# Kernel tuning notes

Hardware: AMD Instinct MI355X
Metric: run time of the kernel (lower is better)

Reference implementation:

```python
import jax, jax.numpy as jnp
import numpy as np

NUM_EXPERTS = 8
TOP_K = 2


def setup_inputs() -> dict:
    key = jax.random.key(0)
    k1, k2, k3, k4, k5 = jax.random.split(key, 5)
    B, S, D, I, E = 1, 2048, 1024, 2816, NUM_EXPERTS
    scale_in = 1.0 / np.sqrt(D)
    scale_mid = 1.0 / np.sqrt(I)
    return {
        "hidden_states": jax.random.normal(k1, (B, S, D), dtype=jnp.float32),
        "w_router": jax.random.normal(k2, (E, D), dtype=jnp.float32) * scale_in,
        "w_gate": jax.random.normal(k3, (E, D, I), dtype=jnp.float32) * scale_in,
        "w_up": jax.random.normal(k4, (E, D, I), dtype=jnp.float32) * scale_in,
        "w_down": jax.random.normal(k5, (E, I, D), dtype=jnp.float32) * scale_mid,
    }


def reference(hidden_states, w_router, w_gate, w_up, w_down):
    B, S, D = hidden_states.shape
    E, K = NUM_EXPERTS, TOP_K
    x = hidden_states.reshape(-1, D)  # (N, D)
    N = x.shape[0]

    # ---- TopKRouter ----
    router_logits = x @ w_router.T                                   # (N, E)
    router_probs = jax.nn.softmax(router_logits.astype(jnp.float32), axis=-1)
    expert_weights, expert_indices = jax.lax.top_k(router_probs, K)  # (N, K)
    # norm_topk_prob = True
    expert_weights = expert_weights / expert_weights.sum(axis=-1, keepdims=True)
    expert_weights = expert_weights.astype(x.dtype)

    # load-balancing aux loss (Switch formulation)
    one_hot = jax.nn.one_hot(expert_indices, E, dtype=jnp.float32)   # (N, K, E)
    tokens_per_expert = one_hot.sum(axis=(0, 1))                     # (E,)
    f = tokens_per_expert / (N * K)
    p = router_probs.mean(axis=0)
    aux_loss = E * jnp.sum(f * p)

    # ---- dropless dispatch/combine ----
    # combine weight per (token, expert): sum of routing weights over slots
    # assigned to that expert (zero for unrouted pairs -> same math as the
    # per-expert gather + index_add_ in the torch code).
    comb = jnp.einsum("nk,nke->ne", expert_weights, one_hot.astype(x.dtype))

    # SwiGLU expert FFN, batched over experts
    g = jnp.einsum("nd,edi->eni", x, w_gate)      # (E, N, I)
    u = jnp.einsum("nd,edi->eni", x, w_up)        # (E, N, I)
    h = jax.nn.silu(g) * u                         # (E, N, I)
    eo = jnp.einsum("eni,eid->end", h, w_down)    # (E, N, D)

    out = jnp.einsum("ne,end->nd", comb, eo)      # (N, D)
    return out.reshape(B, S, D), aux_loss
```

## Files before the change

### kernel.cpp

```cpp
#include <hip/hip_runtime.h>
#include <stdint.h>

#define N_TOK 2048
#define DM 1024
#define DI 2816
#define NE 8
#define NSLOT (N_TOK * 2)
#define BKP 72
#define MAXRT 40
#define NBLK (N_TOK / 4)

typedef __bf16 bf16x8 __attribute__((ext_vector_type(8)));
typedef float f32x4 __attribute__((ext_vector_type(4)));

__device__ __forceinline__ unsigned short f2bf(float f) {
    unsigned u = __builtin_bit_cast(unsigned, f);
    u += 0x7fffu + ((u >> 16) & 1u);
    return (unsigned short)(u >> 16);
}
__device__ __forceinline__ unsigned pack2bf(float a, float b) {
    return (unsigned)f2bf(a) | ((unsigned)f2bf(b) << 16);
}

__device__ __forceinline__ f32x4 mfma_bf16(bf16x8 a, bf16x8 b, f32x4 c) {
    return __builtin_amdgcn_mfma_f32_16x16x32_bf16(a, b, c, 0, 0, 0);
}

__global__ __launch_bounds__(256) void k_router(
    const float* __restrict__ x, const float* __restrict__ wr,
    float* __restrict__ probsum, int* __restrict__ te, float* __restrict__ tw,
    unsigned* __restrict__ hist)
{
    __shared__ int te_s[8];
    __shared__ float ps[4][NE];
    int w = threadIdx.x >> 6, lane = threadIdx.x & 63;
    int n = blockIdx.x * 4 + w;
    const float* xr = x + (size_t)n * DM;

    float acc[NE];
#pragma unroll
    for (int e = 0; e < NE; e++) acc[e] = 0.f;
#pragma unroll
    for (int it = 0; it < DM / 64; it++) {
        float xv = xr[lane + it * 64];
#pragma unroll
        for (int e = 0; e < NE; e++) acc[e] += xv * wr[e * DM + lane + it * 64];
    }
#pragma unroll
    for (int e = 0; e < NE; e++) {
        float v = acc[e];
#pragma unroll
        for (int off = 32; off; off >>= 1) v += __shfl_xor(v, off);
        acc[e] = v;
    }
    float m = acc[0];
#pragma unroll
    for (int e = 1; e < NE; e++) m = fmaxf(m, acc[e]);
    float p[NE], s = 0.f;
#pragma unroll
    for (int e = 0; e < NE; e++) { p[e] = __expf(acc[e] - m); s += p[e]; }
    float inv = 1.f / s;
#pragma unroll
    for (int e = 0; e < NE; e++) p[e] *= inv;
    int i0 = 0;
#pragma unroll
    for (int e = 1; e < NE; e++) if (p[e] > p[i0]) i0 = e;
    int i1 = (i0 == 0) ? 1 : 0;
#pragma unroll
    for (int e = 0; e < NE; e++) if (e != i0 && p[e] > p[i1]) i1 = e;
    float w0 = p[i0] / (p[i0] + p[i1]);
    float w1 = 1.f - w0;

    if (lane == 0) {
        te[2 * n] = i0; te[2 * n + 1] = i1;
        tw[2 * n] = w0; tw[2 * n + 1] = w1;
        te_s[2 * w] = i0; te_s[2 * w + 1] = i1;
    }
    if (lane < NE) ps[w][lane] = p[lane];
    __syncthreads();

    if (threadIdx.x < NE) {
        float s4 = ps[0][threadIdx.x] + ps[1][threadIdx.x] +
                   ps[2][threadIdx.x] + ps[3][threadIdx.x];
        atomicAdd(&probsum[threadIdx.x], s4);
    }
    if (w == 0) {
        unsigned v = 0;
        if (lane < NE) {
            int c = 0;
#pragma unroll
            for (int i = 0; i < 8; i++) c += (te_s[i] == lane);
            v = (unsigned)c << (4 * lane);
        }
        v |= __shfl_xor(v, 1); v |= __shfl_xor(v, 2); v |= __shfl_xor(v, 4);
        if (lane == 0) hist[blockIdx.x] = v;
    }
}

__global__ __launch_bounds__(512) void k_finalize(
    const unsigned* __restrict__ hist, const float* __restrict__ probsum,
    int* __restrict__ counts, int* __restrict__ base,
    int* __restrict__ nrt_out, unsigned short* __restrict__ rtmap,
    unsigned short* __restrict__ blockoff, float* __restrict__ aux_out)
{
    __shared__ int cnts_s[NE], base_s[NE];
    int tid = threadIdx.x;
    int e = tid >> 6, lane = tid & 63;

    int c[8], t = 0;
#pragma unroll
    for (int j = 0; j < 8; j++) {
        c[j] = (int)((hist[lane * 8 + j] >> (4 * e)) & 15u);
        t += c[j];
    }
    int incl = t;
#pragma unroll
    for (int off = 1; off < 64; off <<= 1) {
        int v = __shfl_up(incl, off);
        if (lane >= off) incl += v;
    }
    int excl = incl - t;
    if (lane == 63) cnts_s[e] = incl;
    __syncthreads();

    if (tid == 0) {
        int b = 0, nrt = 0; float aux = 0.f;
        for (int ee = 0; ee < NE; ee++) {
            int cc = cnts_s[ee];
            base_s[ee] = b;
            base[ee] = b;
            counts[ee] = cc;
            b += cc;
            aux += ((float)cc / (float)(N_TOK * 2)) *
                   (probsum[ee] / (float)N_TOK);
            int nt = (cc + 127) >> 7;
            for (int mt = 0; mt < nt; mt++)
                rtmap[nrt++] = (unsigned short)((ee << 8) | mt);
        }
        nrt_out[0] = nrt;
        aux_out[0] = aux * (float)NE;
    }
    __syncthreads();

    int run = base_s[e] + excl;
#pragma unroll
    for (int j = 0; j < 8; j++) {
        blockoff[(lane * 8 + j) * NE + e] = (unsigned short)run;
        run += c[j];
    }
}

__global__ __launch_bounds__(256) void k_gather(
    const float* __restrict__ x, const int* __restrict__ te,
    const unsigned short* __restrict__ blockoff,
    int* __restrict__ slots, unsigned short* __restrict__ Xg)
{
    __shared__ int te_s[8];
    int w = threadIdx.x >> 6, lane = threadIdx.x & 63;
    int n = blockIdx.x * 4 + w;
    if (lane == 0) {
        te_s[2 * w] = te[2 * n];
        te_s[2 * w + 1] = te[2 * n + 1];
    }
    __syncthreads();
    int s0 = 0, s1 = 0;
    if (lane == 0) {
        int i0 = 2 * w, i1 = 2 * w + 1;
        int e0 = te_s[i0], e1 = te_s[i1];
        int r0 = 0, r1 = 0;
        for (int j = 0; j < i0; j++) r0 += (te_s[j] == e0);
        for (int j = 0; j < i1; j++) r1 += (te_s[j] == e1);
        s0 = blockoff[blockIdx.x * NE + e0] + r0;
        s1 = blockoff[blockIdx.x * NE + e1] + r1;
        slots[2 * n] = s0; slots[2 * n + 1] = s1;
    }
    s0 = __shfl(s0, 0); s1 = __shfl(s1, 0);

    const float4* xr = (const float4*)(x + (size_t)n * DM);
    float4 f0 = xr[lane * 4 + 0], f1 = xr[lane * 4 + 1];
    float4 f2 = xr[lane * 4 + 2], f3 = xr[lane * 4 + 3];
    uint4 lo = make_uint4(pack2bf(f0.x, f0.y), pack2bf(f0.z, f0.w),
                          pack2bf(f1.x, f1.y), pack2bf(f1.z, f1.w));
    uint4 hi = make_uint4(pack2bf(f2.x, f2.y), pack2bf(f2.z, f2.w),
                          pack2bf(f3.x, f3.y), pack2bf(f3.z, f3.w));
    uint4* d0 = (uint4*)(Xg + (size_t)s0 * DM) + lane * 2;
    uint4* d1 = (uint4*)(Xg + (size_t)s1 * DM) + lane * 2;
    d0[0] = lo; d0[1] = hi;
    d1[0] = lo; d1[1] = hi;
}

__global__ __launch_bounds__(256) void k_pack(
    const float* __restrict__ src, unsigned short* __restrict__ dst,
    int R, int C)
{
    __shared__ unsigned short T[64][66];
    const float* s = src + (size_t)blockIdx.z * R * C;
    unsigned short* d = dst + (size_t)blockIdx.z * R * C;
    int r0 = blockIdx.y * 64, c0 = blockIdx.x * 64;
    int t = threadIdx.x;
    int ri = t >> 2, cc = (t & 3) * 16;
    const float4* sp = (const float4*)(s + (size_t)(r0 + ri) * C + c0 + cc);
    float4 f0 = sp[0], f1 = sp[1], f2 = sp[2], f3 = sp[3];
    unsigned short* tp = &T[ri][cc];
    *(unsigned*)(tp + 0)  = pack2bf(f0.x, f0.y);
    *(unsigned*)(tp + 2)  = pack2bf(f0.z, f0.w);
    *(unsigned*)(tp + 4)  = pack2bf(f1.x, f1.y);
    *(unsigned*)(tp + 6)  = pack2bf(f1.z, f1.w);
    *(unsigned*)(tp + 8)  = pack2bf(f2.x, f2.y);
    *(unsigned*)(tp + 10) = pack2bf(f2.z, f2.w);
    *(unsigned*)(tp + 12) = pack2bf(f3.x, f3.y);
    *(unsigned*)(tp + 14) = pack2bf(f3.z, f3.w);
    __syncthreads();
    int co = t >> 2, rr = (t & 3) * 16;
    unsigned w0 = (unsigned)T[rr + 0][co] | ((unsigned)T[rr + 1][co] << 16);
    unsigned w1 = (unsigned)T[rr + 2][co] | ((unsigned)T[rr + 3][co] << 16);
    unsigned w2 = (unsigned)T[rr + 4][co] | ((unsigned)T[rr + 5][co] << 16);
    unsigned w3 = (unsigned)T[rr + 6][co] | ((unsigned)T[rr + 7][co] << 16);
    unsigned w4 = (unsigned)T[rr + 8][co] | ((unsigned)T[rr + 9][co] << 16);
    unsigned w5 = (unsigned)T[rr + 10][co] | ((unsigned)T[rr + 11][co] << 16);
    unsigned w6 = (unsigned)T[rr + 12][co] | ((unsigned)T[rr + 13][co] << 16);
    unsigned w7 = (unsigned)T[rr + 14][co] | ((unsigned)T[rr + 15][co] << 16);
    unsigned short* dp = d + (size_t)(c0 + co) * R + r0 + rr;
    *(uint4*)(dp + 0) = make_uint4(w0, w1, w2, w3);
    *(uint4*)(dp + 8) = make_uint4(w4, w5, w6, w7);
}

template<bool PK>
__global__ __launch_bounds__(256, 4) void k_ffn1(
    const unsigned short* __restrict__ Xg,
    const float* __restrict__ wg, const float* __restrict__ wu,
    const unsigned short* __restrict__ wgp, const unsigned short* __restrict__ wup,
    const int* __restrict__ counts, const int* __restrict__ base,
    const int* __restrict__ nrt_p, const unsigned short* __restrict__ rtmap,
    unsigned short* __restrict__ H)
{
    __shared__ unsigned short As[128 * BKP];
    __shared__ unsigned short Bg[64 * BKP];
    __shared__ unsigned short Bu[64 * BKP];

    int tid = threadIdx.x;
    int w = tid >> 6, lane = tid & 63, quad = lane >> 4, ln = lane & 15;
    int ar = tid >> 1;
    int ak = (tid & 1) * 32;
    int kp = tid >> 3, n0 = (tid & 7) * 8;
    int kpsw2 = ((((kp >> 2) ^ (tid & 7)) << 2) | (kp & 3)) * 2;
    int nb = tid >> 2;
    int cA = (tid & 3) * 2;
    int boff0 = nb * BKP + ((cA ^ ((nb >> 3) & 7)) * 8);
    int boff1 = nb * BKP + (((cA + 1) ^ ((nb >> 3) & 7)) * 8);
    int bsrc = cA * 8;

    const int NCT = DI / 64;
    int total = nrt_p[0] * NCT;

    for (int tix = blockIdx.x; tix < total; tix += gridDim.x) {
        int rt = tix / NCT;
        int nc0 = (tix - rt * NCT) * 64;
        int em = rtmap[rt];
        int e = em >> 8, mt = em & 255;
        int cnt = counts[e];
        int row0 = base[e] + mt * 128;
        int rowEnd = base[e] + cnt;
        int arow = row0 + ar; if (arow > NSLOT - 1) arow = NSLOT - 1;

        f32x4 aG[2][4], aU[2][4];
        const f32x4 z = {0.f, 0.f, 0.f, 0.f};
#pragma unroll
        for (int i = 0; i < 2; i++)
#pragma unroll
            for (int j = 0; j < 4; j++) { aG[i][j] = z; aU[i][j] = z; }

        if constexpr (PK) {
            const unsigned short* wgpe = wgp + (size_t)e * DM * DI + (size_t)(nc0 + nb) * DM + bsrc;
            const unsigned short* wupe = wup + (size_t)e * DM * DI + (size_t)(nc0 + nb) * DM + bsrc;
            uint4 pa0, pa1, pa2, pa3, qg0, qg1, qu0, qu1;
            {
                const uint4* a_ = (const uint4*)(Xg + (size_t)arow * DM + ak);
                pa0 = a_[0]; pa1 = a_[1]; pa2 = a_[2]; pa3 = a_[3];
                qg0 = *(const uint4*)(wgpe);     qg1 = *(const uint4*)(wgpe + 8);
                qu0 = *(const uint4*)(wupe);     qu1 = *(const uint4*)(wupe + 8);
            }
            for (int kt = 0; kt < DM / 64; kt++) {
                *(uint4*)&As[ar * BKP + ak + 0]  = pa0;
                *(uint4*)&As[ar * BKP + ak + 8]  = pa1;
                *(uint4*)&As[ar * BKP + ak + 16] = pa2;
                *(uint4*)&As[ar * BKP + ak + 24] = pa3;
                *(uint4*)&Bg[boff0] = qg0;  *(uint4*)&Bg[boff1] = qg1;
                *(uint4*)&Bu[boff0] = qu0;  *(uint4*)&Bu[boff1] = qu1;
                __syncthreads();
                if (kt + 1 < DM / 64) {
                    int k0 = (kt + 1) * 64;
                    const uint4* a_ = (const uint4*)(Xg + (size_t)arow * DM + k0 + ak);
                    pa0 = a_[0]; pa1 = a_[1]; pa2 = a_[2]; pa3 = a_[3];
                    qg0 = *(const uint4*)(wgpe + k0);     qg1 = *(const uint4*)(wgpe + k0 + 8);
                    qu0 = *(const uint4*)(wupe + k0);     qu1 = *(const uint4*)(wupe + k0 + 8);
                }
#pragma unroll
                for (int s = 0; s < 2; s++) {
                    bf16x8 a0 = *(const bf16x8*)&As[(w * 32 + ln) * BKP + s * 32 + quad * 8];
                    bf16x8 a1 = *(const bf16x8*)&As[(w * 32 + 16 + ln) * BKP + s * 32 + quad * 8];
#pragma unroll
                    for (int j = 0; j < 4; j++) {
                        int nn = j * 16 + ln;
                        int grp = (s * 4 + quad) ^ ((nn >> 3) & 7);
                        bf16x8 bg = *(const bf16x8*)&Bg[nn * BKP + grp * 8];
                        bf16x8 bu = *(const bf16x8*)&Bu[nn * BKP + grp * 8];
                        aG[0][j] = mfma_bf16(a0, bg, aG[0][j]);
                        aG[1][j] = mfma_bf16(a1, bg, aG[1][j]);
                        aU[0][j] = mfma_bf16(a0, bu, aU[0][j]);
                        aU[1][j] = mfma_bf16(a1, bu, aU[1][j]);
                    }
                }
                __syncthreads();
            }
        } else {
            const float* wge = wg + (size_t)e * DM * DI;
            const float* wue = wu + (size_t)e * DM * DI;
            for (int kt = 0; kt < DM / 64; kt++) {
                int k0 = kt * 64;
                const uint4* asrc = (const uint4*)(Xg + (size_t)arow * DM + k0 + ak);
                uint4 av0 = asrc[0], av1 = asrc[1], av2 = asrc[2], av3 = asrc[3];
                const float* p0 = wge + (size_t)(k0 + 2 * kp) * DI + nc0 + n0;
                float4 g0 = *(const float4*)(p0),      g1 = *(const float4*)(p0 + 4);
                float4 g2 = *(const float4*)(p0 + DI), g3 = *(const float4*)(p0 + DI + 4);
                const float* p1 = wue + (size_t)(k0 + 2 * kp) * DI + nc0 + n0;
                float4 u0 = *(const float4*)(p1),      u1 = *(const float4*)(p1 + 4);
                float4 u2 = *(const float4*)(p1 + DI), u3 = *(const float4*)(p1 + DI + 4);
                *(uint4*)&As[ar * BKP + ak + 0]  = av0;
                *(uint4*)&As[ar * BKP + ak + 8]  = av1;
                *(uint4*)&As[ar * BKP + ak + 16] = av2;
                *(uint4*)&As[ar * BKP + ak + 24] = av3;
                unsigned short* bg = &Bg[n0 * BKP + kpsw2];
                unsigned short* bu = &Bu[n0 * BKP + kpsw2];
                *(unsigned*)(bg + 0 * BKP) = pack2bf(g0.x, g2.x);
                *(unsigned*)(bg + 1 * BKP) = pack2bf(g0.y, g2.y);
                *(unsigned*)(bg + 2 * BKP) = pack2bf(g0.z, g2.z);
                *(unsigned*)(bg + 3 * BKP) = pack2bf(g0.w, g2.w);
                *(unsigned*)(bg + 4 * BKP) = pack2bf(g1.x, g3.x);
                *(unsigned*)(bg + 5 * BKP) = pack2bf(g1.y, g3.y);
                *(unsigned*)(bg + 6 * BKP) = pack2bf(g1.z, g3.z);
                *(unsigned*)(bg + 7 * BKP) = pack2bf(g1.w, g3.w);
                *(unsigned*)(bu + 0 * BKP) = pack2bf(u0.x, u2.x);
                *(unsigned*)(bu + 1 * BKP) = pack2bf(u0.y, u2.y);
                *(unsigned*)(bu + 2 * BKP) = pack2bf(u0.z, u2.z);
                *(unsigned*)(bu + 3 * BKP) = pack2bf(u0.w, u2.w);
                *(unsigned*)(bu + 4 * BKP) = pack2bf(u1.x, u3.x);
                *(unsigned*)(bu + 5 * BKP) = pack2bf(u1.y, u3.y);
                *(unsigned*)(bu + 6 * BKP) = pack2bf(u1.z, u3.z);
                *(unsigned*)(bu + 7 * BKP) = pack2bf(u1.w, u3.w);
                __syncthreads();
#pragma unroll
                for (int s = 0; s < 2; s++) {
                    bf16x8 a0 = *(const bf16x8*)&As[(w * 32 + ln) * BKP + s * 32 + quad * 8];
                    bf16x8 a1 = *(const bf16x8*)&As[(w * 32 + 16 + ln) * BKP + s * 32 + quad * 8];
#pragma unroll
                    for (int j = 0; j < 4; j++) {
                        int nn = j * 16 + ln;
                        int grp = (s * 4 + quad) ^ ((nn >> 3) & 7);
                        bf16x8 bg8 = *(const bf16x8*)&Bg[nn * BKP + grp * 8];
                        bf16x8 bu8 = *(const bf16x8*)&Bu[nn * BKP + grp * 8];
                        aG[0][j] = mfma_bf16(a0, bg8, aG[0][j]);
                        aG[1][j] = mfma_bf16(a1, bg8, aG[1][j]);
                        aU[0][j] = mfma_bf16(a0, bu8, aU[0][j]);
                        aU[1][j] = mfma_bf16(a1, bu8, aU[1][j]);
                    }
                }
                __syncthreads();
            }
        }
#pragma unroll
        for (int i = 0; i < 2; i++)
#pragma unroll
            for (int r = 0; r < 4; r++) {
                int rl = w * 32 + i * 16 + quad * 4 + r;
                int grow = row0 + rl;
                if (grow < rowEnd) {
                    unsigned short* hp = H + (size_t)grow * DI + nc0 + ln;
#pragma unroll
                    for (int j = 0; j < 4; j++) {
                        float g = aG[i][j][r], u = aU[i][j][r];
                        float h = g * u / (1.f + __expf(-g));
                        hp[j * 16] = f2bf(h);
                    }
                }
            }
    }
}

template<bool PK>
__global__ __launch_bounds__(256, 4) void k_ffn2(
    const unsigned short* __restrict__ H, const float* __restrict__ wd,
    const unsigned short* __restrict__ wdp,
    const int* __restrict__ counts, const int* __restrict__ base,
    const int* __restrict__ nrt_p, const unsigned short* __restrict__ rtmap,
    float* __restrict__ O)
{
    __shared__ unsigned short As[128 * BKP];
    __shared__ unsigned short Bd[64 * BKP];

    int tid = threadIdx.x;
    int w = tid >> 6, lane = tid & 63, quad = lane >> 4, ln = lane & 15;
    int ar = tid >> 1;
    int ak = (tid & 1) * 32;
    int kp = tid >> 3, n0 = (tid & 7) * 8;
    int kpsw2 = ((((kp >> 2) ^ (tid & 7)) << 2) | (kp & 3)) * 2;
    int nb = tid >> 2;
    int cA = (tid & 3) * 2;
    int boff0 = nb * BKP + ((cA ^ ((nb >> 3) & 7)) * 8);
    int boff1 = nb * BKP + (((cA + 1) ^ ((nb >> 3) & 7)) * 8);
    int bsrc = cA * 8;

    const int NCT = DM / 64;
    int total = nrt_p[0] * NCT;

    for (int tix = blockIdx.x; tix < total; tix += gridDim.x) {
        int rt = tix >> 4;
        int nc0 = (tix & 15) * 64;
        int em = rtmap[rt];
        int e = em >> 8, mt = em & 255;
        int cnt = counts[e];
        int row0 = base[e] + mt * 128;
        int rowEnd = base[e] + cnt;
        int arow = row0 + ar; if (arow > NSLOT - 1) arow = NSLOT - 1;

        f32x4 acc[2][4];
        const f32x4 z = {0.f, 0.f, 0.f, 0.f};
#pragma unroll
        for (int i = 0; i < 2; i++)
#pragma unroll
            for (int j = 0; j < 4; j++) acc[i][j] = z;

        if constexpr (PK) {
            const unsigned short* wdpe = wdp + (size_t)e * DM * DI + (size_t)(nc0 + nb) * DI + bsrc;
            uint4 pa0, pa1, pa2, pa3, qd0, qd1;
            {
                const uint4* a_ = (const uint4*)(H + (size_t)arow * DI + ak);
                pa0 = a_[0]; pa1 = a_[1]; pa2 = a_[2]; pa3 = a_[3];
                qd0 = *(const uint4*)(wdpe);  qd1 = *(const uint4*)(wdpe + 8);
            }
            for (int kt = 0; kt < DI / 64; kt++) {
                *(uint4*)&As[ar * BKP + ak + 0]  = pa0;
                *(uint4*)&As[ar * BKP + ak + 8]  = pa1;
                *(uint4*)&As[ar * BKP + ak + 16] = pa2;
                *(uint4*)&As[ar * BKP + ak + 24] = pa3;
                *(uint4*)&Bd[boff0] = qd0;  *(uint4*)&Bd[boff1] = qd1;
                __syncthreads();
                if (kt + 1 < DI / 64) {
                    int k0 = (kt + 1) * 64;
                    const uint4* a_ = (const uint4*)(H + (size_t)arow * DI + k0 + ak);
                    pa0 = a_[0]; pa1 = a_[1]; pa2 = a_[2]; pa3 = a_[3];
                    qd0 = *(const uint4*)(wdpe + k0);  qd1 = *(const uint4*)(wdpe + k0 + 8);
                }
#pragma unroll
                for (int s = 0; s < 2; s++) {
                    bf16x8 a0 = *(const bf16x8*)&As[(w * 32 + ln) * BKP + s * 32 + quad * 8];
                    bf16x8 a1 = *(const bf16x8*)&As[(w * 32 + 16 + ln) * BKP + s * 32 + quad * 8];
#pragma unroll
                    for (int j = 0; j < 4; j++) {
                        int nn = j * 16 + ln;
                        int grp = (s * 4 + quad) ^ ((nn >> 3) & 7);
                        bf16x8 bd = *(const bf16x8*)&Bd[nn * BKP + grp * 8];
                        acc[0][j] = mfma_bf16(a0, bd, acc[0][j]);
                        acc[1][j] = mfma_bf16(a1, bd, acc[1][j]);
                    }
                }
                __syncthreads();
            }
        } else {
            const float* wde = wd + (size_t)e * DI * DM;
            for (int kt = 0; kt < DI / 64; kt++) {
                int k0 = kt * 64;
                const uint4* asrc = (const uint4*)(H + (size_t)arow * DI + k0 + ak);
                uint4 av0 = asrc[0], av1 = asrc[1], av2 = asrc[2], av3 = asrc[3];
                const float* p0 = wde + (size_t)(k0 + 2 * kp) * DM + nc0 + n0;
                float4 d0 = *(const float4*)(p0),      d1 = *(const float4*)(p0 + 4);
                float4 d2 = *(const float4*)(p0 + DM), d3 = *(const float4*)(p0 + DM + 4);
                *(uint4*)&As[ar * BKP + ak + 0]  = av0;
                *(uint4*)&As[ar * BKP + ak + 8]  = av1;
                *(uint4*)&As[ar * BKP + ak + 16] = av2;
                *(uint4*)&As[ar * BKP + ak + 24] = av3;
                unsigned short* bd = &Bd[n0 * BKP + kpsw2];
                *(unsigned*)(bd + 0 * BKP) = pack2bf(d0.x, d2.x);
                *(unsigned*)(bd + 1 * BKP) = pack2bf(d0.y, d2.y);
                *(unsigned*)(bd + 2 * BKP) = pack2bf(d0.z, d2.z);
                *(unsigned*)(bd + 3 * BKP) = pack2bf(d0.w, d2.w);
                *(unsigned*)(bd + 4 * BKP) = pack2bf(d1.x, d3.x);
                *(unsigned*)(bd + 5 * BKP) = pack2bf(d1.y, d3.y);
                *(unsigned*)(bd + 6 * BKP) = pack2bf(d1.z, d3.z);
                *(unsigned*)(bd + 7 * BKP) = pack2bf(d1.w, d3.w);
                __syncthreads();
#pragma unroll
                for (int s = 0; s < 2; s++) {
                    bf16x8 a0 = *(const bf16x8*)&As[(w * 32 + ln) * BKP + s * 32 + quad * 8];
                    bf16x8 a1 = *(const bf16x8*)&As[(w * 32 + 16 + ln) * BKP + s * 32 + quad * 8];
#pragma unroll
                    for (int j = 0; j < 4; j++) {
                        int nn = j * 16 + ln;
                        int grp = (s * 4 + quad) ^ ((nn >> 3) & 7);
                        bf16x8 bd8 = *(const bf16x8*)&Bd[nn * BKP + grp * 8];
                        acc[0][j] = mfma_bf16(a0, bd8, acc[0][j]);
                        acc[1][j] = mfma_bf16(a1, bd8, acc[1][j]);
                    }
                }
                __syncthreads();
            }
        }
#pragma unroll
        for (int i = 0; i < 2; i++)
#pragma unroll
            for (int r = 0; r < 4; r++) {
                int rl = w * 32 + i * 16 + quad * 4 + r;
                int grow = row0 + rl;
                if (grow < rowEnd) {
                    float* op = O + (size_t)grow * DM + nc0 + ln;
#pragma unroll
                    for (int j = 0; j < 4; j++) op[j * 16] = acc[i][j][r];
                }
            }
    }
}

__global__ __launch_bounds__(256) void k_combine(
    const float* __restrict__ O, const int* __restrict__ slots,
    const float* __restrict__ tw, float* __restrict__ out)
{
    int n = blockIdx.x;
    int s0 = slots[2 * n], s1 = slots[2 * n + 1];
    float w0 = tw[2 * n], w1 = tw[2 * n + 1];
    const float4* o0 = (const float4*)(O + (size_t)s0 * DM);
    const float4* o1 = (const float4*)(O + (size_t)s1 * DM);
    float4 a = o0[threadIdx.x], b = o1[threadIdx.x];
    float4 r;
    r.x = w0 * a.x + w1 * b.x;
    r.y = w0 * a.y + w1 * b.y;
    r.z = w0 * a.z + w1 * b.z;
    r.w = w0 * a.w + w1 * b.w;
    ((float4*)(out + (size_t)n * DM))[threadIdx.x] = r;
}

extern "C" void kernel_launch(void* const* d_in, const int* in_sizes, int n_in,
                              void* d_out, int out_size, void* d_ws, size_t ws_size,
                              hipStream_t stream)
{
    const float* x  = (const float*)d_in[0];
    const float* wr = (const float*)d_in[1];
    const float* wg = (const float*)d_in[2];
    const float* wu = (const float*)d_in[3];
    const float* wd = (const float*)d_in[4];
    float* out = (float*)d_out;

    char* ws = (char*)d_ws;
    int*   counts  = (int*)(ws + 0);
    float* probsum = (float*)(ws + 64);
    int*   base    = (int*)(ws + 96);
    int*   nrt     = (int*)(ws + 128);
    unsigned short* rtmap = (unsigned short*)(ws + 132);
    int*   te      = (int*)(ws + 256);
    float* tw      = (float*)(ws + 256 + 16384);
    int*   slots   = (int*)(ws + 256 + 32768);

    size_t off_Xg = 49408;
    size_t off_Hb = off_Xg + (size_t)NSLOT * DM * 2;
    size_t off_O  = off_Hb + (size_t)NSLOT * DI * 2;
    size_t off_Wg = off_O + (size_t)NSLOT * DM * 4;
    size_t off_Wu = off_Wg + (size_t)NE * DM * DI * 2;
    size_t off_Wd = off_Wu + (size_t)NE * DM * DI * 2;
    size_t end_GU = off_Wd;
    size_t end_D  = off_Wd + (size_t)NE * DM * DI * 2;

    unsigned short* Xg  = (unsigned short*)(ws + off_Xg);
    unsigned short* Hb  = (unsigned short*)(ws + off_Hb);
    float*          O   = (float*)(ws + off_O);
    unsigned short* Wgp = (unsigned short*)(ws + off_Wg);
    unsigned short* Wup = (unsigned short*)(ws + off_Wu);
    unsigned short* Wdp = (unsigned short*)(ws + off_Wd);

    unsigned*       hist     = (unsigned*)(ws + off_O);
    unsigned short* blockoff = (unsigned short*)(ws + off_O + 4096);

    bool pkGU = ws_size >= end_GU;
    bool pkD  = ws_size >= end_D;

    hipMemsetAsync(ws, 0, 128, stream);
    k_router<<<NBLK, 256, 0, stream>>>(x, wr, probsum, te, tw, hist);
    k_finalize<<<1, 512, 0, stream>>>(hist, probsum, counts, base, nrt, rtmap,
                                      blockoff, out + (size_t)N_TOK * DM);
    k_gather<<<NBLK, 256, 0, stream>>>(x, te, blockoff, slots, Xg);

    if (pkGU) {
        k_pack<<<dim3(DI / 64, DM / 64, NE), 256, 0, stream>>>(wg, Wgp, DM, DI);
        k_pack<<<dim3(DI / 64, DM / 64, NE), 256, 0, stream>>>(wu, Wup, DM, DI);
    }
    if (pkD)
        k_pack<<<dim3(DM / 64, DI / 64, NE), 256, 0, stream>>>(wd, Wdp, DI, DM);

    if (pkGU)
        k_ffn1<true><<<MAXRT * (DI / 64), 256, 0, stream>>>(
            Xg, wg, wu, Wgp, Wup, counts, base, nrt, rtmap, Hb);
    else
        k_ffn1<false><<<MAXRT * (DI / 64), 256, 0, stream>>>(
            Xg, wg, wu, Wgp, Wup, counts, base, nrt, rtmap, Hb);

    if (pkD)
        k_ffn2<true><<<MAXRT * (DM / 64), 256, 0, stream>>>(
            Hb, wd, Wdp, counts, base, nrt, rtmap, O);
    else
        k_ffn2<false><<<MAXRT * (DM / 64), 256, 0, stream>>>(
            Hb, wd, Wdp, counts, base, nrt, rtmap, O);

    k_combine<<<N_TOK, 256, 0, stream>>>(O, slots, tw, out);
}
```

Before: 465.5 us.

## Fuse gate/up weight packing and remap FFN tile order for XCD locality

Merges the two gate/up weight pack launches into one grid with a doubled z dimension, saving a launch and its tail. In both FFN kernels the tile index now runs over row tiles fastest within each column tile. Block IDs are also remapped so that each group of consecutive block IDs (round-robined across the 8 XCDs) lands on a contiguous tile range. The aim is that blocks sharing a weight column tile run on the same XCD and reuse its L2, at the cost of an extra integer divide per tile.

```diff
diff --git a/kernel.cpp b/kernel.cpp
--- a/kernel.cpp
+++ b/kernel.cpp
@@ -189,13 +189,10 @@
     d1[0] = lo; d1[1] = hi;
 }
 
-__global__ __launch_bounds__(256) void k_pack(
-    const float* __restrict__ src, unsigned short* __restrict__ dst,
-    int R, int C)
+__device__ __forceinline__ void pack_body(
+    const float* __restrict__ s, unsigned short* __restrict__ d, int R, int C)
 {
     __shared__ unsigned short T[64][66];
-    const float* s = src + (size_t)blockIdx.z * R * C;
-    unsigned short* d = dst + (size_t)blockIdx.z * R * C;
     int r0 = blockIdx.y * 64, c0 = blockIdx.x * 64;
     int t = threadIdx.x;
     int ri = t >> 2, cc = (t & 3) * 16;
@@ -225,6 +222,25 @@
     *(uint4*)(dp + 8) = make_uint4(w4, w5, w6, w7);
 }
 
+__global__ __launch_bounds__(256) void k_pack(
+    const float* __restrict__ src, unsigned short* __restrict__ dst,
+    int R, int C)
+{
+    pack_body(src + (size_t)blockIdx.z * R * C,
+              dst + (size_t)blockIdx.z * R * C, R, C);
+}
+
+__global__ __launch_bounds__(256) void k_pack2(
+    const float* __restrict__ srcA, unsigned short* __restrict__ dstA,
+    const float* __restrict__ srcB, unsigned short* __restrict__ dstB,
+    int R, int C)
+{
+    int z = blockIdx.z;
+    const float* s = (z < NE ? srcA : srcB) + (size_t)(z & 7) * R * C;
+    unsigned short* d = (z < NE ? dstA : dstB) + (size_t)(z & 7) * R * C;
+    pack_body(s, d, R, C);
+}
+
 template<bool PK>
 __global__ __launch_bounds__(256, 4) void k_ffn1(
     const unsigned short* __restrict__ Xg,
@@ -251,11 +267,14 @@
     int bsrc = cA * 8;
 
     const int NCT = DI / 64;
-    int total = nrt_p[0] * NCT;
-
-    for (int tix = blockIdx.x; tix < total; tix += gridDim.x) {
-        int rt = tix / NCT;
-        int nc0 = (tix - rt * NCT) * 64;
+    int nrt_v = nrt_p[0];
+    int total = nrt_v * NCT;
+    int wgid = (blockIdx.x & 7) * (gridDim.x >> 3) + (blockIdx.x >> 3);
+
+    for (int tix = wgid; tix < total; tix += gridDim.x) {
+        int nc = tix / nrt_v;
+        int rt = tix - nc * nrt_v;
+        int nc0 = nc * 64;
         int em = rtmap[rt];
         int e = em >> 8, mt = em & 255;
         int cnt = counts[e];
@@ -411,11 +430,14 @@
     int bsrc = cA * 8;
 
     const int NCT = DM / 64;
-    int total = nrt_p[0] * NCT;
-
-    for (int tix = blockIdx.x; tix < total; tix += gridDim.x) {
-        int rt = tix >> 4;
-        int nc0 = (tix & 15) * 64;
+    int nrt_v = nrt_p[0];
+    int total = nrt_v * NCT;
+    int wgid = (blockIdx.x & 7) * (gridDim.x >> 3) + (blockIdx.x >> 3);
+
+    for (int tix = wgid; tix < total; tix += gridDim.x) {
+        int nc = tix / nrt_v;
+        int rt = tix - nc * nrt_v;
+        int nc0 = nc * 64;
         int em = rtmap[rt];
         int e = em >> 8, mt = em & 255;
         int cnt = counts[e];
@@ -587,10 +609,9 @@
                                       blockoff, out + (size_t)N_TOK * DM);
     k_gather<<<NBLK, 256, 0, stream>>>(x, te, blockoff, slots, Xg);
 
-    if (pkGU) {
-        k_pack<<<dim3(DI / 64, DM / 64, NE), 256, 0, stream>>>(wg, Wgp, DM, DI);
-        k_pack<<<dim3(DI / 64, DM / 64, NE), 256, 0, stream>>>(wu, Wup, DM, DI);
-    }
+    if (pkGU)
+        k_pack2<<<dim3(DI / 64, DM / 64, 2 * NE), 256, 0, stream>>>(
+            wg, Wgp, wu, Wup, DM, DI);
     if (pkD)
         k_pack<<<dim3(DM / 64, DI / 64, NE), 256, 0, stream>>>(wd, Wdp, DI, DM);
 
```

Measured after the change: 474.1 us. About the same (+1.8%).

## Drop weight pre-pack kernels and convert fp32 weights inside the GEMM loops

Applied to the files above, without the earlier changes.

Removes the three k_pack launches that transposed and converted the gate, up and down weights to bf16 in the workspace, along with the templated packed paths. The FFN kernels now always read fp32 weights directly and convert them to bf16 while staging into shared memory. This avoids a full extra read and write pass over all expert weights on every call. In exchange, each GEMM tile reads twice the bytes and loses the register prefetch double-buffering the packed path had.

```diff
diff --git a/kernel.cpp b/kernel.cpp
--- a/kernel.cpp
+++ b/kernel.cpp
@@ -189,47 +189,9 @@
     d1[0] = lo; d1[1] = hi;
 }
 
-__global__ __launch_bounds__(256) void k_pack(
-    const float* __restrict__ src, unsigned short* __restrict__ dst,
-    int R, int C)
-{
-    __shared__ unsigned short T[64][66];
-    const float* s = src + (size_t)blockIdx.z * R * C;
-    unsigned short* d = dst + (size_t)blockIdx.z * R * C;
-    int r0 = blockIdx.y * 64, c0 = blockIdx.x * 64;
-    int t = threadIdx.x;
-    int ri = t >> 2, cc = (t & 3) * 16;
-    const float4* sp = (const float4*)(s + (size_t)(r0 + ri) * C + c0 + cc);
-    float4 f0 = sp[0], f1 = sp[1], f2 = sp[2], f3 = sp[3];
-    unsigned short* tp = &T[ri][cc];
-    *(unsigned*)(tp + 0)  = pack2bf(f0.x, f0.y);
-    *(unsigned*)(tp + 2)  = pack2bf(f0.z, f0.w);
-    *(unsigned*)(tp + 4)  = pack2bf(f1.x, f1.y);
-    *(unsigned*)(tp + 6)  = pack2bf(f1.z, f1.w);
-    *(unsigned*)(tp + 8)  = pack2bf(f2.x, f2.y);
-    *(unsigned*)(tp + 10) = pack2bf(f2.z, f2.w);
-    *(unsigned*)(tp + 12) = pack2bf(f3.x, f3.y);
-    *(unsigned*)(tp + 14) = pack2bf(f3.z, f3.w);
-    __syncthreads();
-    int co = t >> 2, rr = (t & 3) * 16;
-    unsigned w0 = (unsigned)T[rr + 0][co] | ((unsigned)T[rr + 1][co] << 16);
-    unsigned w1 = (unsigned)T[rr + 2][co] | ((unsigned)T[rr + 3][co] << 16);
-    unsigned w2 = (unsigned)T[rr + 4][co] | ((unsigned)T[rr + 5][co] << 16);
-    unsigned w3 = (unsigned)T[rr + 6][co] | ((unsigned)T[rr + 7][co] << 16);
-    unsigned w4 = (unsigned)T[rr + 8][co] | ((unsigned)T[rr + 9][co] << 16);
-    unsigned w5 = (unsigned)T[rr + 10][co] | ((unsigned)T[rr + 11][co] << 16);
-    unsigned w6 = (unsigned)T[rr + 12][co] | ((unsigned)T[rr + 13][co] << 16);
-    unsigned w7 = (unsigned)T[rr + 14][co] | ((unsigned)T[rr + 15][co] << 16);
-    unsigned short* dp = d + (size_t)(c0 + co) * R + r0 + rr;
-    *(uint4*)(dp + 0) = make_uint4(w0, w1, w2, w3);
-    *(uint4*)(dp + 8) = make_uint4(w4, w5, w6, w7);
-}
-
-template<bool PK>
 __global__ __launch_bounds__(256, 4) void k_ffn1(
     const unsigned short* __restrict__ Xg,
     const float* __restrict__ wg, const float* __restrict__ wu,
-    const unsigned short* __restrict__ wgp, const unsigned short* __restrict__ wup,
     const int* __restrict__ counts, const int* __restrict__ base,
     const int* __restrict__ nrt_p, const unsigned short* __restrict__ rtmap,
     unsigned short* __restrict__ H)
@@ -244,11 +206,6 @@
     int ak = (tid & 1) * 32;
     int kp = tid >> 3, n0 = (tid & 7) * 8;
     int kpsw2 = ((((kp >> 2) ^ (tid & 7)) << 2) | (kp & 3)) * 2;
-    int nb = tid >> 2;
-    int cA = (tid & 3) * 2;
-    int boff0 = nb * BKP + ((cA ^ ((nb >> 3) & 7)) * 8);
-    int boff1 = nb * BKP + (((cA + 1) ^ ((nb >> 3) & 7)) * 8);
-    int bsrc = cA * 8;
 
     const int NCT = DI / 64;
     int total = nrt_p[0] * NCT;
@@ -270,103 +227,58 @@
 #pragma unroll
             for (int j = 0; j < 4; j++) { aG[i][j] = z; aU[i][j] = z; }
 
-        if constexpr (PK) {
-            const unsigned short* wgpe = wgp + (size_t)e * DM * DI + (size_t)(nc0 + nb) * DM + bsrc;
-            const unsigned short* wupe = wup + (size_t)e * DM * DI + (size_t)(nc0 + nb) * DM + bsrc;
-            uint4 pa0, pa1, pa2, pa3, qg0, qg1, qu0, qu1;
-            {
-                const uint4* a_ = (const uint4*)(Xg + (size_t)arow * DM + ak);
-                pa0 = a_[0]; pa1 = a_[1]; pa2 = a_[2]; pa3 = a_[3];
-                qg0 = *(const uint4*)(wgpe);     qg1 = *(const uint4*)(wgpe + 8);
-                qu0 = *(const uint4*)(wupe);     qu1 = *(const uint4*)(wupe + 8);
+        const float* wge = wg + (size_t)e * DM * DI;
+        const float* wue = wu + (size_t)e * DM * DI;
+        for (int kt = 0; kt < DM / 64; kt++) {
+            int k0 = kt * 64;
+            const uint4* asrc = (const uint4*)(Xg + (size_t)arow * DM + k0 + ak);
+            uint4 av0 = asrc[0], av1 = asrc[1], av2 = asrc[2], av3 = asrc[3];
+            const float* p0 = wge + (size_t)(k0 + 2 * kp) * DI + nc0 + n0;
+            float4 g0 = *(const float4*)(p0),      g1 = *(const float4*)(p0 + 4);
+            float4 g2 = *(const float4*)(p0 + DI), g3 = *(const float4*)(p0 + DI + 4);
+            const float* p1 = wue + (size_t)(k0 + 2 * kp) * DI + nc0 + n0;
+            float4 u0 = *(const float4*)(p1),      u1 = *(const float4*)(p1 + 4);
+            float4 u2 = *(const float4*)(p1 + DI), u3 = *(const float4*)(p1 + DI + 4);
+            *(uint4*)&As[ar * BKP + ak + 0]  = av0;
+            *(uint4*)&As[ar * BKP + ak + 8]  = av1;
+            *(uint4*)&As[ar * BKP + ak + 16] = av2;
+            *(uint4*)&As[ar * BKP + ak + 24] = av3;
+            unsigned short* bg = &Bg[n0 * BKP + kpsw2];
+            unsigned short* bu = &Bu[n0 * BKP + kpsw2];
+            *(unsigned*)(bg + 0 * BKP) = pack2bf(g0.x, g2.x);
+            *(unsigned*)(bg + 1 * BKP) = pack2bf(g0.y, g2.y);
+            *(unsigned*)(bg + 2 * BKP) = pack2bf(g0.z, g2.z);
+            *(unsigned*)(bg + 3 * BKP) = pack2bf(g0.w, g2.w);
+            *(unsigned*)(bg + 4 * BKP) = pack2bf(g1.x, g3.x);
+            *(unsigned*)(bg + 5 * BKP) = pack2bf(g1.y, g3.y);
+            *(unsigned*)(bg + 6 * BKP) = pack2bf(g1.z, g3.z);
+            *(unsigned*)(bg + 7 * BKP) = pack2bf(g1.w, g3.w);
+            *(unsigned*)(bu + 0 * BKP) = pack2bf(u0.x, u2.x);
+            *(unsigned*)(bu + 1 * BKP) = pack2bf(u0.y, u2.y);
+            *(unsigned*)(bu + 2 * BKP) = pack2bf(u0.z, u2.z);
+            *(unsigned*)(bu + 3 * BKP) = pack2bf(u0.w, u2.w);
+            *(unsigned*)(bu + 4 * BKP) = pack2bf(u1.x, u3.x);
+            *(unsigned*)(bu + 5 * BKP) = pack2bf(u1.y, u3.y);
+            *(unsigned*)(bu + 6 * BKP) = pack2bf(u1.z, u3.z);
+            *(unsigned*)(bu + 7 * BKP) = pack2bf(u1.w, u3.w);
+            __syncthreads();
+#pragma unroll
+            for (int s = 0; s < 2; s++) {
+                bf16x8 a0 = *(const bf16x8*)&As[(w * 32 + ln) * BKP + s * 32 + quad * 8];
+                bf16x8 a1 = *(const bf16x8*)&As[(w * 32 + 16 + ln) * BKP + s * 32 + quad * 8];
+#pragma unroll
+                for (int j = 0; j < 4; j++) {
+                    int nn = j * 16 + ln;
+                    int grp = (s * 4 + quad) ^ ((nn >> 3) & 7);
+                    bf16x8 bg8 = *(const bf16x8*)&Bg[nn * BKP + grp * 8];
+                    bf16x8 bu8 = *(const bf16x8*)&Bu[nn * BKP + grp * 8];
+                    aG[0][j] = mfma_bf16(a0, bg8, aG[0][j]);
+                    aG[1][j] = mfma_bf16(a1, bg8, aG[1][j]);
+                    aU[0][j] = mfma_bf16(a0, bu8, aU[0][j]);
+                    aU[1][j] = mfma_bf16(a1, bu8, aU[1][j]);
+                }
             }
-            for (int kt = 0; kt < DM / 64; kt++) {
-                *(uint4*)&As[ar * BKP + ak + 0]  = pa0;
-                *(uint4*)&As[ar * BKP + ak + 8]  = pa1;
-                *(uint4*)&As[ar * BKP + ak + 16] = pa2;
-                *(uint4*)&As[ar * BKP + ak + 24] = pa3;
-                *(uint4*)&Bg[boff0] = qg0;  *(uint4*)&Bg[boff1] = qg1;
-                *(uint4*)&Bu[boff0] = qu0;  *(uint4*)&Bu[boff1] = qu1;
-                __syncthreads();
-                if (kt + 1 < DM / 64) {
-                    int k0 = (kt + 1) * 64;
-                    const uint4* a_ = (const uint4*)(Xg + (size_t)arow * DM + k0 + ak);
-                    pa0 = a_[0]; pa1 = a_[1]; pa2 = a_[2]; pa3 = a_[3];
-                    qg0 = *(const uint4*)(wgpe + k0);     qg1 = *(const uint4*)(wgpe + k0 + 8);
-                    qu0 = *(const uint4*)(wupe + k0);     qu1 = *(const uint4*)(wupe + k0 + 8);
-                }
-#pragma unroll
-                for (int s = 0; s < 2; s++) {
-                    bf16x8 a0 = *(const bf16x8*)&As[(w * 32 + ln) * BKP + s * 32 + quad * 8];
-                    bf16x8 a1 = *(const bf16x8*)&As[(w * 32 + 16 + ln) * BKP + s * 32 + quad * 8];
-#pragma unroll
-                    for (int j = 0; j < 4; j++) {
-                        int nn = j * 16 + ln;
-                        int grp = (s * 4 + quad) ^ ((nn >> 3) & 7);
-                        bf16x8 bg = *(const bf16x8*)&Bg[nn * BKP + grp * 8];
-                        bf16x8 bu = *(const bf16x8*)&Bu[nn * BKP + grp * 8];
-                        aG[0][j] = mfma_bf16(a0, bg, aG[0][j]);
-                        aG[1][j] = mfma_bf16(a1, bg, aG[1][j]);
-                        aU[0][j] = mfma_bf16(a0, bu, aU[0][j]);
-                        aU[1][j] = mfma_bf16(a1, bu, aU[1][j]);
-                    }
-                }
-                __syncthreads();
-            }
-        } else {
-            const float* wge = wg + (size_t)e * DM * DI;
-            const float* wue = wu + (size_t)e * DM * DI;
-            for (int kt = 0; kt < DM / 64; kt++) {
-                int k0 = kt * 64;
-                const uint4* asrc = (const uint4*)(Xg + (size_t)arow * DM + k0 + ak);
-                uint4 av0 = asrc[0], av1 = asrc[1], av2 = asrc[2], av3 = asrc[3];
-                const float* p0 = wge + (size_t)(k0 + 2 * kp) * DI + nc0 + n0;
-                float4 g0 = *(const float4*)(p0),      g1 = *(const float4*)(p0 + 4);
-                float4 g2 = *(const float4*)(p0 + DI), g3 = *(const float4*)(p0 + DI + 4);
-                const float* p1 = wue + (size_t)(k0 + 2 * kp) * DI + nc0 + n0;
-                float4 u0 = *(const float4*)(p1),      u1 = *(const float4*)(p1 + 4);
-                float4 u2 = *(const float4*)(p1 + DI), u3 = *(const float4*)(p1 + DI + 4);
-                *(uint4*)&As[ar * BKP + ak + 0]  = av0;
-                *(uint4*)&As[ar * BKP + ak + 8]  = av1;
-                *(uint4*)&As[ar * BKP + ak + 16] = av2;
-                *(uint4*)&As[ar * BKP + ak + 24] = av3;
-                unsigned short* bg = &Bg[n0 * BKP + kpsw2];
-                unsigned short* bu = &Bu[n0 * BKP + kpsw2];
-                *(unsigned*)(bg + 0 * BKP) = pack2bf(g0.x, g2.x);
-                *(unsigned*)(bg + 1 * BKP) = pack2bf(g0.y, g2.y);
-                *(unsigned*)(bg + 2 * BKP) = pack2bf(g0.z, g2.z);
-                *(unsigned*)(bg + 3 * BKP) = pack2bf(g0.w, g2.w);
-                *(unsigned*)(bg + 4 * BKP) = pack2bf(g1.x, g3.x);
-                *(unsigned*)(bg + 5 * BKP) = pack2bf(g1.y, g3.y);
-                *(unsigned*)(bg + 6 * BKP) = pack2bf(g1.z, g3.z);
-                *(unsigned*)(bg + 7 * BKP) = pack2bf(g1.w, g3.w);
-                *(unsigned*)(bu + 0 * BKP) = pack2bf(u0.x, u2.x);
-                *(unsigned*)(bu + 1 * BKP) = pack2bf(u0.y, u2.y);
-                *(unsigned*)(bu + 2 * BKP) = pack2bf(u0.z, u2.z);
-                *(unsigned*)(bu + 3 * BKP) = pack2bf(u0.w, u2.w);
-                *(unsigned*)(bu + 4 * BKP) = pack2bf(u1.x, u3.x);
-                *(unsigned*)(bu + 5 * BKP) = pack2bf(u1.y, u3.y);
-                *(unsigned*)(bu + 6 * BKP) = pack2bf(u1.z, u3.z);
-                *(unsigned*)(bu + 7 * BKP) = pack2bf(u1.w, u3.w);
-                __syncthreads();
-#pragma unroll
-                for (int s = 0; s < 2; s++) {
-                    bf16x8 a0 = *(const bf16x8*)&As[(w * 32 + ln) * BKP + s * 32 + quad * 8];
-                    bf16x8 a1 = *(const bf16x8*)&As[(w * 32 + 16 + ln) * BKP + s * 32 + quad * 8];
-#pragma unroll
-                    for (int j = 0; j < 4; j++) {
-                        int nn = j * 16 + ln;
-                        int grp = (s * 4 + quad) ^ ((nn >> 3) & 7);
-                        bf16x8 bg8 = *(const bf16x8*)&Bg[nn * BKP + grp * 8];
-                        bf16x8 bu8 = *(const bf16x8*)&Bu[nn * BKP + grp * 8];
-                        aG[0][j] = mfma_bf16(a0, bg8, aG[0][j]);
-                        aG[1][j] = mfma_bf16(a1, bg8, aG[1][j]);
-                        aU[0][j] = mfma_bf16(a0, bu8, aU[0][j]);
-                        aU[1][j] = mfma_bf16(a1, bu8, aU[1][j]);
-                    }
-                }
-                __syncthreads();
-            }
+            __syncthreads();
         }
 #pragma unroll
         for (int i = 0; i < 2; i++)
@@ -387,10 +299,8 @@
     }
 }
 
-template<bool PK>
 __global__ __launch_bounds__(256, 4) void k_ffn2(
     const unsigned short* __restrict__ H, const float* __restrict__ wd,
-    const unsigned short* __restrict__ wdp,
     const int* __restrict__ counts, const int* __restrict__ base,
     const int* __restrict__ nrt_p, const unsigned short* __restrict__ rtmap,
     float* __restrict__ O)
@@ -404,11 +314,6 @@
     int ak = (tid & 1) * 32;
     int kp = tid >> 3, n0 = (tid & 7) * 8;
     int kpsw2 = ((((kp >> 2) ^ (tid & 7)) << 2) | (kp & 3)) * 2;
-    int nb = tid >> 2;
-    int cA = (tid & 3) * 2;
-    int boff0 = nb * BKP + ((cA ^ ((nb >> 3) & 7)) * 8);
-    int boff1 = nb * BKP + (((cA + 1) ^ ((nb >> 3) & 7)) * 8);
-    int bsrc = cA * 8;
 
     const int NCT = DM / 64;
     int total = nrt_p[0] * NCT;
@@ -430,80 +335,42 @@
 #pragma unroll
             for (int j = 0; j < 4; j++) acc[i][j] = z;
 
-        if constexpr (PK) {
-            const unsigned short* wdpe = wdp + (size_t)e * DM * DI + (size_t)(nc0 + nb) * DI + bsrc;
-            uint4 pa0, pa1, pa2, pa3, qd0, qd1;
-            {
-                const uint4* a_ = (const uint4*)(H + (size_t)arow * DI + ak);
-                pa0 = a_[0]; pa1 = a_[1]; pa2 = a_[2]; pa3 = a_[3];
-                qd0 = *(const uint4*)(wdpe);  qd1 = *(const uint4*)(wdpe + 8);
+        const float* wde = wd + (size_t)e * DI * DM;
+        for (int kt = 0; kt < DI / 64; kt++) {
+            int k0 = kt * 64;
+            const uint4* asrc = (const uint4*)(H + (size_t)arow * DI + k0 + ak);
+            uint4 av0 = asrc[0], av1 = asrc[1], av2 = asrc[2], av3 = asrc[3];
+            const float* p0 = wde + (size_t)(k0 + 2 * kp) * DM + nc0 + n0;
+            float4 d0 = *(const float4*)(p0),      d1 = *(const float4*)(p0 + 4);
+            float4 d2 = *(const float4*)(p0 + DM), d3 = *(const float4*)(p0 + DM + 4);
+            *(uint4*)&As[ar * BKP + ak + 0]  = av0;
+            *(uint4*)&As[ar * BKP + ak + 8]  = av1;
+            *(uint4*)&As[ar * BKP + ak + 16] = av2;
+            *(uint4*)&As[ar * BKP + ak + 24] = av3;
+            unsigned short* bd = &Bd[n0 * BKP + kpsw2];
+            *(unsigned*)(bd + 0 * BKP) = pack2bf(d0.x, d2.x);
+            *(unsigned*)(bd + 1 * BKP) = pack2bf(d0.y, d2.y);
+            *(unsigned*)(bd + 2 * BKP) = pack2bf(d0.z, d2.z);
+            *(unsigned*)(bd + 3 * BKP) = pack2bf(d0.w, d2.w);
+            *(unsigned*)(bd + 4 * BKP) = pack2bf(d1.x, d3.x);
+            *(unsigned*)(bd + 5 * BKP) = pack2bf(d1.y, d3.y);
+            *(unsigned*)(bd + 6 * BKP) = pack2bf(d1.z, d3.z);
+            *(unsigned*)(bd + 7 * BKP) = pack2bf(d1.w, d3.w);
+            __syncthreads();
+#pragma unroll
+            for (int s = 0; s < 2; s++) {
+                bf16x8 a0 = *(const bf16x8*)&As[(w * 32 + ln) * BKP + s * 32 + quad * 8];
+                bf16x8 a1 = *(const bf16x8*)&As[(w * 32 + 16 + ln) * BKP + s * 32 + quad * 8];
+#pragma unroll
+                for (int j = 0; j < 4; j++) {
+                    int nn = j * 16 + ln;
+                    int grp = (s * 4 + quad) ^ ((nn >> 3) & 7);
+                    bf16x8 bd8 = *(const bf16x8*)&Bd[nn * BKP + grp * 8];
+                    acc[0][j] = mfma_bf16(a0, bd8, acc[0][j]);
+                    acc[1][j] = mfma_bf16(a1, bd8, acc[1][j]);
+                }
             }
-            for (int kt = 0; kt < DI / 64; kt++) {
-                *(uint4*)&As[ar * BKP + ak + 0]  = pa0;
-                *(uint4*)&As[ar * BKP + ak + 8]  = pa1;
-                *(uint4*)&As[ar * BKP + ak + 16] = pa2;
-                *(uint4*)&As[ar * BKP + ak + 24] = pa3;
-                *(uint4*)&Bd[boff0] = qd0;  *(uint4*)&Bd[boff1] = qd1;
-                __syncthreads();
-                if (kt + 1 < DI / 64) {
-                    int k0 = (kt + 1) * 64;
-                    const uint4* a_ = (const uint4*)(H + (size_t)arow * DI + k0 + ak);
-                    pa0 = a_[0]; pa1 = a_[1]; pa2 = a_[2]; pa3 = a_[3];
-                    qd0 = *(const uint4*)(wdpe + k0);  qd1 = *(const uint4*)(wdpe + k0 + 8);
-                }
-#pragma unroll
-                for (int s = 0; s < 2; s++) {
-                    bf16x8 a0 = *(const bf16x8*)&As[(w * 32 + ln) * BKP + s * 32 + quad * 8];
-                    bf16x8 a1 = *(const bf16x8*)&As[(w * 32 + 16 + ln) * BKP + s * 32 + quad * 8];
-#pragma unroll
-                    for (int j = 0; j < 4; j++) {
-                        int nn = j * 16 + ln;
-                        int grp = (s * 4 + quad) ^ ((nn >> 3) & 7);
-                        bf16x8 bd = *(const bf16x8*)&Bd[nn * BKP + grp * 8];
-                        acc[0][j] = mfma_bf16(a0, bd, acc[0][j]);
-                        acc[1][j] = mfma_bf16(a1, bd, acc[1][j]);
-                    }
-                }
-                __syncthreads();
-            }
-        } else {
-            const float* wde = wd + (size_t)e * DI * DM;
-            for (int kt = 0; kt < DI / 64; kt++) {
-                int k0 = kt * 64;
-                const uint4* asrc = (const uint4*)(H + (size_t)arow * DI + k0 + ak);
-                uint4 av0 = asrc[0], av1 = asrc[1], av2 = asrc[2], av3 = asrc[3];
-                const float* p0 = wde + (size_t)(k0 + 2 * kp) * DM + nc0 + n0;
-                float4 d0 = *(const float4*)(p0),      d1 = *(const float4*)(p0 + 4);
-                float4 d2 = *(const float4*)(p0 + DM), d3 = *(const float4*)(p0 + DM + 4);
-                *(uint4*)&As[ar * BKP + ak + 0]  = av0;
-                *(uint4*)&As[ar * BKP + ak + 8]  = av1;
-                *(uint4*)&As[ar * BKP + ak + 16] = av2;
-                *(uint4*)&As[ar * BKP + ak + 24] = av3;
-                unsigned short* bd = &Bd[n0 * BKP + kpsw2];
-                *(unsigned*)(bd + 0 * BKP) = pack2bf(d0.x, d2.x);
-                *(unsigned*)(bd + 1 * BKP) = pack2bf(d0.y, d2.y);
-                *(unsigned*)(bd + 2 * BKP) = pack2bf(d0.z, d2.z);
-                *(unsigned*)(bd + 3 * BKP) = pack2bf(d0.w, d2.w);
-                *(unsigned*)(bd + 4 * BKP) = pack2bf(d1.x, d3.x);
-                *(unsigned*)(bd + 5 * BKP) = pack2bf(d1.y, d3.y);
-                *(unsigned*)(bd + 6 * BKP) = pack2bf(d1.z, d3.z);
-                *(unsigned*)(bd + 7 * BKP) = pack2bf(d1.w, d3.w);
-                __syncthreads();
-#pragma unroll
-                for (int s = 0; s < 2; s++) {
-                    bf16x8 a0 = *(const bf16x8*)&As[(w * 32 + ln) * BKP + s * 32 + quad * 8];
-                    bf16x8 a1 = *(const bf16x8*)&As[(w * 32 + 16 + ln) * BKP + s * 32 + quad * 8];
-#pragma unroll
-                    for (int j = 0; j < 4; j++) {
-                        int nn = j * 16 + ln;
-                        int grp = (s * 4 + quad) ^ ((nn >> 3) & 7);
-                        bf16x8 bd8 = *(const bf16x8*)&Bd[nn * BKP + grp * 8];
-                        acc[0][j] = mfma_bf16(a0, bd8, acc[0][j]);
-                        acc[1][j] = mfma_bf16(a1, bd8, acc[1][j]);
-                    }
-                }
-                __syncthreads();
-            }
+            __syncthreads();
         }
 #pragma unroll
         for (int i = 0; i < 2; i++)
@@ -562,24 +429,13 @@
     size_t off_Xg = 49408;
     size_t off_Hb = off_Xg + (size_t)NSLOT * DM * 2;
     size_t off_O  = off_Hb + (size_t)NSLOT * DI * 2;
-    size_t off_Wg = off_O + (size_t)NSLOT * DM * 4;
-    size_t off_Wu = off_Wg + (size_t)NE * DM * DI * 2;
-    size_t off_Wd = off_Wu + (size_t)NE * DM * DI * 2;
-    size_t end_GU = off_Wd;
-    size_t end_D  = off_Wd + (size_t)NE * DM * DI * 2;
 
     unsigned short* Xg  = (unsigned short*)(ws + off_Xg);
     unsigned short* Hb  = (unsigned short*)(ws + off_Hb);
     float*          O   = (float*)(ws + off_O);
-    unsigned short* Wgp = (unsigned short*)(ws + off_Wg);
-    unsigned short* Wup = (unsigned short*)(ws + off_Wu);
-    unsigned short* Wdp = (unsigned short*)(ws + off_Wd);
 
     unsigned*       hist     = (unsigned*)(ws + off_O);
     unsigned short* blockoff = (unsigned short*)(ws + off_O + 4096);
-
-    bool pkGU = ws_size >= end_GU;
-    bool pkD  = ws_size >= end_D;
 
     hipMemsetAsync(ws, 0, 128, stream);
     k_router<<<NBLK, 256, 0, stream>>>(x, wr, probsum, te, tw, hist);
@@ -587,26 +443,10 @@
                                       blockoff, out + (size_t)N_TOK * DM);
     k_gather<<<NBLK, 256, 0, stream>>>(x, te, blockoff, slots, Xg);
 
-    if (pkGU) {
-        k_pack<<<dim3(DI / 64, DM / 64, NE), 256, 0, stream>>>(wg, Wgp, DM, DI);
-        k_pack<<<dim3(DI / 64, DM / 64, NE), 256, 0, stream>>>(wu, Wup, DM, DI);
-    }
-    if (pkD)
-        k_pack<<<dim3(DM / 64, DI / 64, NE), 256, 0, stream>>>(wd, Wdp, DI, DM);
-
-    if (pkGU)
-        k_ffn1<true><<<MAXRT * (DI / 64), 256, 0, stream>>>(
-            Xg, wg, wu, Wgp, Wup, counts, base, nrt, rtmap, Hb);
-    else
-        k_ffn1<false><<<MAXRT * (DI / 64), 256, 0, stream>>>(
-            Xg, wg, wu, Wgp, Wup, counts, base, nrt, rtmap, Hb);
-
-    if (pkD)
-        k_ffn2<true><<<MAXRT * (DM / 64), 256, 0, stream>>>(
-            Hb, wd, Wdp, counts, base, nrt, rtmap, O);
-    else
-        k_ffn2<false><<<MAXRT * (DM / 64), 256, 0, stream>>>(
-            Hb, wd, Wdp, counts, base, nrt, rtmap, O);
+    k_ffn1<<<MAXRT * (DI / 64), 256, 0, stream>>>(
+        Xg, wg, wu, counts, base, nrt, rtmap, Hb);
+    k_ffn2<<<MAXRT * (DM / 64), 256, 0, stream>>>(
+        Hb, wd, counts, base, nrt, rtmap, O);
 
     k_combine<<<N_TOK, 256, 0, stream>>>(O, slots, tw, out);
 }
```

New measurement: 458.8 us. About the same (-1.4%).
